# Performance work log

Measured on AMD Instinct MI355X. Metric: run time of the kernel, lower is better.

The kernel has to match this reference:

```python
import jax, jax.numpy as jnp
import numpy as np

N_NODES = 50000
N_EDGES = 800000
IN_FEATS = 96
HIDDEN = 96
OUT_FEATS = 8


def setup_inputs() -> dict:
    key = jax.random.key(0)
    k = jax.random.split(key, 10)
    features = jax.random.normal(k[0], (N_NODES, IN_FEATS), dtype=jnp.float32)
    src = jax.random.randint(k[1], (N_EDGES,), 0, N_NODES, dtype=jnp.int32)
    dst = jax.random.randint(k[2], (N_EDGES,), 0, N_NODES, dtype=jnp.int32)
    # DGL GraphConv weights: shape (in, out), xavier-uniform; bias zeros (we use small randn for nontrivial grads)
    def glorot(kk, fan_in, fan_out):
        lim = np.sqrt(6.0 / (fan_in + fan_out))
        return jax.random.uniform(kk, (fan_in, fan_out), jnp.float32, -lim, lim)
    W1 = glorot(k[3], IN_FEATS, HIDDEN)
    b1 = jnp.zeros((HIDDEN,), jnp.float32)
    W2 = glorot(k[4], HIDDEN, HIDDEN)
    b2 = jnp.zeros((HIDDEN,), jnp.float32)
    # torch Linear readout: weight [out, in], bias [out]
    Wr = glorot(k[5], OUT_FEATS, HIDDEN)
    br = jnp.zeros((OUT_FEATS,), jnp.float32)
    return {"features": features, "src": src, "dst": dst,
            "W1": W1, "b1": b1, "W2": W2, "b2": b2, "Wr": Wr, "br": br}


def _degree_norms(src, dst, n_nodes):
    ones = jnp.ones(src.shape[0], jnp.float32)
    deg_out = jax.ops.segment_sum(ones, src, num_segments=n_nodes)
    deg_in = jax.ops.segment_sum(ones, dst, num_segments=n_nodes)
    norm_out = jnp.clip(deg_out, 1.0, None) ** -0.5  # D_out^{-1/2}
    norm_in = jnp.clip(deg_in, 1.0, None) ** -0.5    # D_in^{-1/2}
    return norm_out, norm_in


def _graph_conv(x, src, dst, norm_out, norm_in, W, b):
    # DGL GraphConv, norm='both': scale src feats, sum-aggregate over edges,
    # scale by in-degree norm, dense transform + bias.
    x = x * norm_out[:, None]
    msgs = x[src]                                           # [E, d] gather
    agg = jax.ops.segment_sum(msgs, dst, num_segments=x.shape[0])  # [N, d] scatter-add
    agg = agg * norm_in[:, None]
    return agg @ W + b


def reference(features, src, dst, W1, b1, W2, b2, Wr, br):
    n = features.shape[0]
    norm_out, norm_in = _degree_norms(src, dst, n)
    x = jax.nn.relu(_graph_conv(features, src, dst, norm_out, norm_in, W1, b1))
    x = _graph_conv(x, src, dst, norm_out, norm_in, W2, b2)
    hg = jnp.mean(x, axis=0, keepdims=True)  # [1, hidden]
    return hg @ Wr.T + br                    # [1, out_feats]
```

## Files before the change

### kernel.cpp

```cpp
#include <hip/hip_runtime.h>


constexpr int NN = 50000;
constexpr int NE = 800000;
constexpr int NB = 196;
constexpr int CAP = 6144;

constexpr int OFF_SVEC     = 0;
constexpr int OFF_BCURD    = 256;
constexpr int OFF_BCURS    = 3392;
constexpr int OFF_NORM_OUT = 6528;
constexpr int OFF_NORM_IN  = 56528;
constexpr int OFF_CW       = 106528;
constexpr int OFF_ROW_PTR  = 156528;
constexpr int OFF_EDGE_SRC = 206532;
constexpr int OFF_PD       = 606532;
constexpr int OFF_PS       = 1810756;
constexpr int OFF_YP       = 606532;
constexpr size_t ZERO_BYTES = (size_t)(OFF_NORM_OUT) * 4;

__global__ __launch_bounds__(256)
void k_part(const int* __restrict__ src, const int* __restrict__ dst,
            int* __restrict__ bcur_d, int* __restrict__ bcur_s,
            int* __restrict__ pd, int* __restrict__ ps) {
  __shared__ int hd[256], hs[256], gd[256], gs[256];
  __shared__ int ldx[256], cur[256], scn[256];
  __shared__ int stage[2048];
  __shared__ unsigned char stageB[2048];
  const int t = threadIdx.x;
  hd[t] = 0; hs[t] = 0;
  __syncthreads();
  const int e0 = blockIdx.x * 2048;
  int s_[8], d_[8];
#pragma unroll
  for (int i = 0; i < 8; ++i) {
    int e = e0 + i * 256 + t;
    bool v = e < NE;
    s_[i] = v ? src[e] : -1;
    d_[i] = v ? dst[e] : -1;
    if (v) { atomicAdd(&hd[d_[i] >> 8], 1); atomicAdd(&hs[s_[i] >> 8], 1); }
  }
  __syncthreads();
  if (t < NB) {
    int c = hd[t];
    gd[t] = c ? (t * CAP + atomicAdd(&bcur_d[t * 16], c)) : 0;
    c = hs[t];
    gs[t] = c ? (t * CAP + atomicAdd(&bcur_s[t * 16], c)) : 0;
  }

  scn[t] = hd[t];
  __syncthreads();
  for (int off = 1; off < 256; off <<= 1) {
    int u = (t >= off) ? scn[t - off] : 0;
    __syncthreads();
    scn[t] += u;
    __syncthreads();
  }
  ldx[t] = scn[t] - hd[t];
  cur[t] = scn[t] - hd[t];
  const int totd = scn[255];
  __syncthreads();
#pragma unroll
  for (int i = 0; i < 8; ++i) {
    if (d_[i] >= 0) {
      int B = d_[i] >> 8;
      int p = atomicAdd(&cur[B], 1);
      stage[p] = (s_[i] << 8) | (d_[i] & 255);
      stageB[p] = (unsigned char)B;
    }
  }
  __syncthreads();
  for (int j = t; j < totd; j += 256) {
    int B = stageB[j];
    pd[gd[B] + (j - ldx[B])] = stage[j];
  }
  __syncthreads();

  scn[t] = hs[t];
  __syncthreads();
  for (int off = 1; off < 256; off <<= 1) {
    int u = (t >= off) ? scn[t - off] : 0;
    __syncthreads();
    scn[t] += u;
    __syncthreads();
  }
  ldx[t] = scn[t] - hs[t];
  cur[t] = scn[t] - hs[t];
  const int tots = scn[255];
  __syncthreads();
#pragma unroll
  for (int i = 0; i < 8; ++i) {
    if (s_[i] >= 0) {
      int B = s_[i] >> 8;
      int p = atomicAdd(&cur[B], 1);
      stage[p] = (d_[i] << 8) | (s_[i] & 255);
      stageB[p] = (unsigned char)B;
    }
  }
  __syncthreads();
  for (int j = t; j < tots; j += 256) {
    int B = stageB[j];
    ps[gs[B] + (j - ldx[B])] = stage[j];
  }
}

__global__ __launch_bounds__(256)
void k_csr(const int* __restrict__ pd, const int* __restrict__ bcur_d,
           int* __restrict__ row_ptr, float* __restrict__ norm_in,
           unsigned short* __restrict__ edge_src) {
  __shared__ int pe_s[CAP];
  __shared__ int hist[256], cur[256], sc[256];
  const int t = threadIdx.x, b = blockIdx.x;
  hist[t] = 0;
  __syncthreads();
  const int cnt = bcur_d[b * 16];
  const int* pe = pd + b * CAP;
  for (int i = t; i < cnt; i += 256) {
    int p = pe[i];
    pe_s[i] = p;
    atomicAdd(&hist[p & 255], 1);
  }

  sc[t] = (t < b) ? bcur_d[t * 16] : 0;
  __syncthreads();
  for (int s = 128; s > 0; s >>= 1) {
    if (t < s) sc[t] += sc[t + s];
    __syncthreads();
  }
  const int base0 = sc[0];
  __syncthreads();

  int h = hist[t];
  sc[t] = h;
  __syncthreads();
  for (int off = 1; off < 256; off <<= 1) {
    int u = (t >= off) ? sc[t - off] : 0;
    __syncthreads();
    sc[t] += u;
    __syncthreads();
  }
  int excl = base0 + sc[t] - h;
  int n = b * 256 + t;
  if (n < NN) {
    row_ptr[n] = excl;
    norm_in[n] = 1.0f / sqrtf((float)max(h, 1));
  }
  cur[t] = excl;
  __syncthreads();
  if (b == NB - 1 && t == 0) row_ptr[NN] = base0 + cnt;

  for (int i = t; i < cnt; i += 256) {
    int p = pe_s[i];
    int pos = atomicAdd(&cur[p & 255], 1);
    edge_src[pos] = (unsigned short)(p >> 8);
  }
}

__global__ __launch_bounds__(256)
void k_bin_src(const int* __restrict__ ps, const int* __restrict__ bcur_s,
               const float* __restrict__ norm_in,
               float* __restrict__ norm_out, float* __restrict__ cw) {
  __shared__ int dout[256];
  __shared__ float craw[256];
  const int t = threadIdx.x, b = blockIdx.x;
  dout[t] = 0; craw[t] = 0.f;
  __syncthreads();
  const int cnt = bcur_s[b * 16];
  const int* pe = ps + b * CAP;
  for (int i = t; i < cnt; i += 256) {
    int p = pe[i];
    atomicAdd(&dout[p & 255], 1);
    atomicAdd(&craw[p & 255], norm_in[p >> 8]);
  }
  __syncthreads();
  int n = b * 256 + t;
  if (n < NN) {
    float no = 1.0f / sqrtf((float)max(dout[t], 1));
    norm_out[n] = no;
    cw[n] = no * craw[t];
  }
}

__global__ __launch_bounds__(256, 6)
void k_xform(const float* __restrict__ feats, const float* __restrict__ norm_out,
             const float* __restrict__ W1, float* __restrict__ YP) {
  __shared__ float XT[96][68];
  const int t = threadIdx.x;
  const int nb = blockIdx.x * 64;

  const float4* f4 = (const float4*)feats;
#pragma unroll
  for (int i = 0; i < 6; ++i) {
    int idx4 = i * 256 + t;
    int n = idx4 / 24;
    int kq = idx4 % 24;
    int ng = nb + n;
    float4 v = make_float4(0.f, 0.f, 0.f, 0.f);
    float no = 0.f;
    if (ng < NN) { v = f4[(size_t)ng * 24 + kq]; no = norm_out[ng]; }
    XT[kq * 4 + 0][n] = v.x * no;
    XT[kq * 4 + 1][n] = v.y * no;
    XT[kq * 4 + 2][n] = v.z * no;
    XT[kq * 4 + 3][n] = v.w * no;
  }
  __syncthreads();

  const int tn = t & 7;
  const int tm = t >> 3;
  float acc0[12], acc1[12];
#pragma unroll
  for (int c = 0; c < 12; ++c) { acc0[c] = 0.f; acc1[c] = 0.f; }

  const float4* W4 = (const float4*)(W1 + 12 * tn);
#pragma unroll 4
  for (int k = 0; k < 96; ++k) {
    float2 x = *(const float2*)&XT[k][2 * tm];
    float4 w0 = W4[k * 24 + 0];
    float4 w1 = W4[k * 24 + 1];
    float4 w2 = W4[k * 24 + 2];
    const float w[12] = {w0.x, w0.y, w0.z, w0.w, w1.x, w1.y, w1.z, w1.w,
                         w2.x, w2.y, w2.z, w2.w};
#pragma unroll
    for (int c = 0; c < 12; ++c) {
      acc0[c] = fmaf(x.x, w[c], acc0[c]);
      acc1[c] = fmaf(x.y, w[c], acc1[c]);
    }
  }

  int n0 = nb + 2 * tm;
#pragma unroll
  for (int c4 = 0; c4 < 3; ++c4) {
    int col = 12 * tn + 4 * c4;
    int p = col >> 4, off = col & 15;
    float* base = YP + ((size_t)p * NN) * 16 + off;
    if (n0 < NN)
      *(float4*)(base + (size_t)n0 * 16) =
          make_float4(acc0[4 * c4], acc0[4 * c4 + 1], acc0[4 * c4 + 2], acc0[4 * c4 + 3]);
    if (n0 + 1 < NN)
      *(float4*)(base + (size_t)(n0 + 1) * 16) =
          make_float4(acc1[4 * c4], acc1[4 * c4 + 1], acc1[4 * c4 + 2], acc1[4 * c4 + 3]);
  }
}

__global__ __launch_bounds__(256, 6)
void k_agg(const float* __restrict__ YP,
           const float* __restrict__ norm_in, const float* __restrict__ cw,
           const int* __restrict__ row_ptr, const unsigned short* __restrict__ edge_src,
           const float* __restrict__ b1, float* __restrict__ svec) {
  __shared__ float red[16];
  const int tid = threadIdx.x;
  if (tid < 16) red[tid] = 0.f;
  __syncthreads();

  const int xcd   = blockIdx.x & 7;
  const int bp    = blockIdx.x >> 3;
  const int panel = (xcd < 6) ? xcd : (xcd - 6);
  const int slotb = (xcd >= 6) ? 256 : 0;
  const int nslot = (panel < 2) ? 512 : 256;
  const int stride = nslot * 8;

  const int g = tid >> 5, l = tid & 31;
  const int ei = l >> 2;
  const int q4 = (l & 3) * 4;

  const float* Yp = YP + (size_t)panel * NN * 16;
  float4 b4 = make_float4(0.f, 0.f, 0.f, 0.f);
  if (l < 4) b4 = ((const float4*)b1)[4 * panel + l];

  float a0 = 0.f, a1 = 0.f, a2 = 0.f, a3 = 0.f;

  const int gid = (slotb + bp) * 8 + g;
  for (int n = gid; n < NN; n += 2 * stride) {
    const int m = n + stride;
    const bool hb = (m < NN);
    int e1a = row_ptr[n + 1], basea = row_ptr[n];
    int e1b = 0, baseb = 0;
    if (hb) { e1b = row_ptr[m + 1]; baseb = row_ptr[m]; }
    float va0 = 0.f, va1 = 0.f, va2 = 0.f, va3 = 0.f;
    float vb0 = 0.f, vb1 = 0.f, vb2 = 0.f, vb3 = 0.f;

    while (basea < e1a || baseb < e1b) {
      int cnta = min(32, e1a - basea);
      int cntb = min(32, e1b - baseb);
      int esa = 0, esb = 0;
      if (basea + l < e1a) esa = edge_src[basea + l] * 16;
      if (baseb + l < e1b) esb = edge_src[baseb + l] * 16;

      if (cnta > 0) {
        int s0 = __shfl(esa, ei, 32);
        float4 f0 = make_float4(0.f, 0.f, 0.f, 0.f);
        if (ei < cnta) f0 = *(const float4*)(Yp + s0 + q4);
        if (cnta > 8) {
          int s1 = __shfl(esa, 8 + ei, 32);
          float4 f1 = make_float4(0.f, 0.f, 0.f, 0.f);
          if (8 + ei < cnta) f1 = *(const float4*)(Yp + s1 + q4);
          f0.x += f1.x; f0.y += f1.y; f0.z += f1.z; f0.w += f1.w;
        }
        if (cnta > 16) {
          int s2 = __shfl(esa, 16 + ei, 32);
          int s3 = __shfl(esa, 24 + ei, 32);
          float4 f2 = make_float4(0.f, 0.f, 0.f, 0.f), f3 = f2;
          if (16 + ei < cnta) f2 = *(const float4*)(Yp + s2 + q4);
          if (24 + ei < cnta) f3 = *(const float4*)(Yp + s3 + q4);
          f0.x += f2.x + f3.x; f0.y += f2.y + f3.y;
          f0.z += f2.z + f3.z; f0.w += f2.w + f3.w;
        }
        va0 += f0.x; va1 += f0.y; va2 += f0.z; va3 += f0.w;
      }
      if (cntb > 0) {
        int s0 = __shfl(esb, ei, 32);
        float4 f0 = make_float4(0.f, 0.f, 0.f, 0.f);
        if (ei < cntb) f0 = *(const float4*)(Yp + s0 + q4);
        if (cntb > 8) {
          int s1 = __shfl(esb, 8 + ei, 32);
          float4 f1 = make_float4(0.f, 0.f, 0.f, 0.f);
          if (8 + ei < cntb) f1 = *(const float4*)(Yp + s1 + q4);
          f0.x += f1.x; f0.y += f1.y; f0.z += f1.z; f0.w += f1.w;
        }
        if (cntb > 16) {
          int s2 = __shfl(esb, 16 + ei, 32);
          int s3 = __shfl(esb, 24 + ei, 32);
          float4 f2 = make_float4(0.f, 0.f, 0.f, 0.f), f3 = f2;
          if (16 + ei < cntb) f2 = *(const float4*)(Yp + s2 + q4);
          if (24 + ei < cntb) f3 = *(const float4*)(Yp + s3 + q4);
          f0.x += f2.x + f3.x; f0.y += f2.y + f3.y;
          f0.z += f2.z + f3.z; f0.w += f2.w + f3.w;
        }
        vb0 += f0.x; vb1 += f0.y; vb2 += f0.z; vb3 += f0.w;
      }
      basea += 32; baseb += 32;
    }

    va0 += __shfl(va0, l + 16, 32); va1 += __shfl(va1, l + 16, 32);
    va2 += __shfl(va2, l + 16, 32); va3 += __shfl(va3, l + 16, 32);
    va0 += __shfl(va0, l + 8, 32);  va1 += __shfl(va1, l + 8, 32);
    va2 += __shfl(va2, l + 8, 32);  va3 += __shfl(va3, l + 8, 32);
    va0 += __shfl(va0, l + 4, 32);  va1 += __shfl(va1, l + 4, 32);
    va2 += __shfl(va2, l + 4, 32);  va3 += __shfl(va3, l + 4, 32);

    vb0 += __shfl(vb0, l + 16, 32); vb1 += __shfl(vb1, l + 16, 32);
    vb2 += __shfl(vb2, l + 16, 32); vb3 += __shfl(vb3, l + 16, 32);
    vb0 += __shfl(vb0, l + 8, 32);  vb1 += __shfl(vb1, l + 8, 32);
    vb2 += __shfl(vb2, l + 8, 32);  vb3 += __shfl(vb3, l + 8, 32);
    vb0 += __shfl(vb0, l + 4, 32);  vb1 += __shfl(vb1, l + 4, 32);
    vb2 += __shfl(vb2, l + 4, 32);  vb3 += __shfl(vb3, l + 4, 32);

    if (l < 4) {
      float ni = norm_in[n], c = cw[n];
      a0 += c * fmaxf(fmaf(ni, va0, b4.x), 0.f);
      a1 += c * fmaxf(fmaf(ni, va1, b4.y), 0.f);
      a2 += c * fmaxf(fmaf(ni, va2, b4.z), 0.f);
      a3 += c * fmaxf(fmaf(ni, va3, b4.w), 0.f);
      if (hb) {
        float nib = norm_in[m], cb = cw[m];
        a0 += cb * fmaxf(fmaf(nib, vb0, b4.x), 0.f);
        a1 += cb * fmaxf(fmaf(nib, vb1, b4.y), 0.f);
        a2 += cb * fmaxf(fmaf(nib, vb2, b4.z), 0.f);
        a3 += cb * fmaxf(fmaf(nib, vb3, b4.w), 0.f);
      }
    }
  }

  if (l < 4) {
    atomicAdd(&red[4 * l + 0], a0);
    atomicAdd(&red[4 * l + 1], a1);
    atomicAdd(&red[4 * l + 2], a2);
    atomicAdd(&red[4 * l + 3], a3);
  }
  __syncthreads();
  if (tid < 16) atomicAdd(&svec[16 * panel + tid], red[tid]);
}

__global__ void k_final(const float* __restrict__ svec,
                        const float* __restrict__ W2, const float* __restrict__ b2,
                        const float* __restrict__ Wr, const float* __restrict__ br,
                        float* __restrict__ out) {
  __shared__ float hg[96];
  int j = threadIdx.x;
  if (j < 96) {
    float acc = b2[j];
    const float invN = 1.0f / (float)NN;
    for (int k = 0; k < 96; ++k)
      acc = fmaf(svec[k] * invN, W2[k * 96 + j], acc);
    hg[j] = acc;
  }
  __syncthreads();
  if (j < 8) {
    float acc = br[j];
    for (int k = 0; k < 96; ++k)
      acc = fmaf(hg[k], Wr[j * 96 + k], acc);
    out[j] = acc;
  }
}

extern "C" void kernel_launch(void* const* d_in, const int* in_sizes, int n_in,
                              void* d_out, int out_size, void* d_ws, size_t ws_size,
                              hipStream_t stream) {
  const float* feats = (const float*)d_in[0];
  const int*   src   = (const int*)d_in[1];
  const int*   dst   = (const int*)d_in[2];
  const float* W1    = (const float*)d_in[3];
  const float* b1    = (const float*)d_in[4];
  const float* W2    = (const float*)d_in[5];
  const float* b2    = (const float*)d_in[6];
  const float* Wr    = (const float*)d_in[7];
  const float* br    = (const float*)d_in[8];
  float* out = (float*)d_out;

  int*   wsi      = (int*)d_ws;
  float* wsf      = (float*)d_ws;
  float* svec     = wsf + OFF_SVEC;
  int*   bcur_d   = wsi + OFF_BCURD;
  int*   bcur_s   = wsi + OFF_BCURS;
  float* norm_out = wsf + OFF_NORM_OUT;
  float* norm_in  = wsf + OFF_NORM_IN;
  float* cw       = wsf + OFF_CW;
  int*   row_ptr  = wsi + OFF_ROW_PTR;
  unsigned short* edge_src = (unsigned short*)(wsi + OFF_EDGE_SRC);
  int*   pd       = wsi + OFF_PD;
  int*   ps       = wsi + OFF_PS;
  float* YP       = wsf + OFF_YP;

  hipMemsetAsync(d_ws, 0, ZERO_BYTES, stream);

  k_part<<<(NE + 2047) / 2048, 256, 0, stream>>>(src, dst, bcur_d, bcur_s, pd, ps);
  k_csr<<<NB, 256, 0, stream>>>(pd, bcur_d, row_ptr, norm_in, edge_src);
  k_bin_src<<<NB, 256, 0, stream>>>(ps, bcur_s, norm_in, norm_out, cw);
  k_xform<<<(NN + 63) / 64, 256, 0, stream>>>(feats, norm_out, W1, YP);
  k_agg<<<2048, 256, 0, stream>>>(YP, norm_in, cw, row_ptr, edge_src, b1, svec);
  k_final<<<1, 128, 0, stream>>>(svec, W2, b2, Wr, br, out);
}
```

Baseline: 219.7 us.

## Aggregate per 256-node bucket with LDS atomic accumulation instead of per-node warp gathers

The aggregation kernel now gives each block one 256-destination bucket for one 16-column panel. Edges are split evenly across 16 slots, and each gathered feature is scatter-added into a padded LDS accumulator using shared atomics. Edge entries are stored as full ints carrying both the source and local destination, which doubles edge array traffic and shifts workspace offsets. This removes per-node load imbalance and the shuffle reductions, at the cost of LDS atomic contention and scalar 4-byte gathers in place of float4 loads.

```diff
diff --git a/kernel.cpp b/kernel.cpp
--- a/kernel.cpp
+++ b/kernel.cpp
@@ -14,9 +14,9 @@
 constexpr int OFF_CW       = 106528;
 constexpr int OFF_ROW_PTR  = 156528;
 constexpr int OFF_EDGE_SRC = 206532;
-constexpr int OFF_PD       = 606532;
-constexpr int OFF_PS       = 1810756;
-constexpr int OFF_YP       = 606532;
+constexpr int OFF_PD       = 1006532;
+constexpr int OFF_PS       = 2210756;
+constexpr int OFF_YP       = 1006532;
 constexpr size_t ZERO_BYTES = (size_t)(OFF_NORM_OUT) * 4;
 
 __global__ __launch_bounds__(256)
@@ -107,7 +107,7 @@
 __global__ __launch_bounds__(256)
 void k_csr(const int* __restrict__ pd, const int* __restrict__ bcur_d,
            int* __restrict__ row_ptr, float* __restrict__ norm_in,
-           unsigned short* __restrict__ edge_src) {
+           int* __restrict__ edge_src) {
   __shared__ int pe_s[CAP];
   __shared__ int hist[256], cur[256], sc[256];
   const int t = threadIdx.x, b = blockIdx.x;
@@ -152,7 +152,7 @@
   for (int i = t; i < cnt; i += 256) {
     int p = pe_s[i];
     int pos = atomicAdd(&cur[p & 255], 1);
-    edge_src[pos] = (unsigned short)(p >> 8);
+    edge_src[pos] = p;
   }
 }
 
@@ -242,133 +242,74 @@
   }
 }
 
-__global__ __launch_bounds__(256, 6)
+__global__ __launch_bounds__(256)
 void k_agg(const float* __restrict__ YP,
            const float* __restrict__ norm_in, const float* __restrict__ cw,
-           const int* __restrict__ row_ptr, const unsigned short* __restrict__ edge_src,
+           const int* __restrict__ row_ptr, const int* __restrict__ edge_src,
            const float* __restrict__ b1, float* __restrict__ svec) {
+  __shared__ float acc[256 * 17];
   __shared__ float red[16];
-  const int tid = threadIdx.x;
-  if (tid < 16) red[tid] = 0.f;
-  __syncthreads();
-
-  const int xcd   = blockIdx.x & 7;
-  const int bp    = blockIdx.x >> 3;
-  const int panel = (xcd < 6) ? xcd : (xcd - 6);
-  const int slotb = (xcd >= 6) ? 256 : 0;
-  const int nslot = (panel < 2) ? 512 : 256;
-  const int stride = nslot * 8;
-
-  const int g = tid >> 5, l = tid & 31;
-  const int ei = l >> 2;
-  const int q4 = (l & 3) * 4;
-
-  const float* Yp = YP + (size_t)panel * NN * 16;
-  float4 b4 = make_float4(0.f, 0.f, 0.f, 0.f);
-  if (l < 4) b4 = ((const float4*)b1)[4 * panel + l];
-
-  float a0 = 0.f, a1 = 0.f, a2 = 0.f, a3 = 0.f;
-
-  const int gid = (slotb + bp) * 8 + g;
-  for (int n = gid; n < NN; n += 2 * stride) {
-    const int m = n + stride;
-    const bool hb = (m < NN);
-    int e1a = row_ptr[n + 1], basea = row_ptr[n];
-    int e1b = 0, baseb = 0;
-    if (hb) { e1b = row_ptr[m + 1]; baseb = row_ptr[m]; }
-    float va0 = 0.f, va1 = 0.f, va2 = 0.f, va3 = 0.f;
-    float vb0 = 0.f, vb1 = 0.f, vb2 = 0.f, vb3 = 0.f;
-
-    while (basea < e1a || baseb < e1b) {
-      int cnta = min(32, e1a - basea);
-      int cntb = min(32, e1b - baseb);
-      int esa = 0, esb = 0;
-      if (basea + l < e1a) esa = edge_src[basea + l] * 16;
-      if (baseb + l < e1b) esb = edge_src[baseb + l] * 16;
-
-      if (cnta > 0) {
-        int s0 = __shfl(esa, ei, 32);
-        float4 f0 = make_float4(0.f, 0.f, 0.f, 0.f);
-        if (ei < cnta) f0 = *(const float4*)(Yp + s0 + q4);
-        if (cnta > 8) {
-          int s1 = __shfl(esa, 8 + ei, 32);
-          float4 f1 = make_float4(0.f, 0.f, 0.f, 0.f);
-          if (8 + ei < cnta) f1 = *(const float4*)(Yp + s1 + q4);
-          f0.x += f1.x; f0.y += f1.y; f0.z += f1.z; f0.w += f1.w;
-        }
-        if (cnta > 16) {
-          int s2 = __shfl(esa, 16 + ei, 32);
-          int s3 = __shfl(esa, 24 + ei, 32);
-          float4 f2 = make_float4(0.f, 0.f, 0.f, 0.f), f3 = f2;
-          if (16 + ei < cnta) f2 = *(const float4*)(Yp + s2 + q4);
-          if (24 + ei < cnta) f3 = *(const float4*)(Yp + s3 + q4);
-          f0.x += f2.x + f3.x; f0.y += f2.y + f3.y;
-          f0.z += f2.z + f3.z; f0.w += f2.w + f3.w;
-        }
-        va0 += f0.x; va1 += f0.y; va2 += f0.z; va3 += f0.w;
-      }
-      if (cntb > 0) {
-        int s0 = __shfl(esb, ei, 32);
-        float4 f0 = make_float4(0.f, 0.f, 0.f, 0.f);
-        if (ei < cntb) f0 = *(const float4*)(Yp + s0 + q4);
-        if (cntb > 8) {
-          int s1 = __shfl(esb, 8 + ei, 32);
-          float4 f1 = make_float4(0.f, 0.f, 0.f, 0.f);
-          if (8 + ei < cntb) f1 = *(const float4*)(Yp + s1 + q4);
-          f0.x += f1.x; f0.y += f1.y; f0.z += f1.z; f0.w += f1.w;
-        }
-        if (cntb > 16) {
-          int s2 = __shfl(esb, 16 + ei, 32);
-          int s3 = __shfl(esb, 24 + ei, 32);
-          float4 f2 = make_float4(0.f, 0.f, 0.f, 0.f), f3 = f2;
-          if (16 + ei < cntb) f2 = *(const float4*)(Yp + s2 + q4);
-          if (24 + ei < cntb) f3 = *(const float4*)(Yp + s3 + q4);
-          f0.x += f2.x + f3.x; f0.y += f2.y + f3.y;
-          f0.z += f2.z + f3.z; f0.w += f2.w + f3.w;
-        }
-        vb0 += f0.x; vb1 += f0.y; vb2 += f0.z; vb3 += f0.w;
-      }
-      basea += 32; baseb += 32;
+  const int t = threadIdx.x;
+  const int x = blockIdx.x & 7, g = blockIdx.x >> 3;
+  int panel, bucket;
+  if (x < 6) {
+    panel = x;
+    if (x < 2) { if (g >= 98) return; bucket = 2 * g; }
+    else       { bucket = g; }
+  } else {
+    panel = x - 6;
+    if (g >= 98) return;
+    bucket = 2 * g + 1;
+  }
+
+  for (int i = t; i < 256 * 17; i += 256) acc[i] = 0.f;
+  if (t < 16) red[t] = 0.f;
+  __syncthreads();
+
+  const int nb = bucket * 256;
+  const int e0 = row_ptr[nb];
+  const int e1 = row_ptr[min(nb + 256, NN)];
+  const float* __restrict__ Yp = YP + (size_t)panel * NN * 16;
+
+  const int slot = t >> 4, col = t & 15;
+  const int cnt = e1 - e0;
+  const int L = (cnt + 15) >> 4;
+  const int i0 = e0 + slot * L;
+  const int iend = min(i0 + L, e1);
+#pragma unroll 4
+  for (int i = i0; i < iend; ++i) {
+    int p = edge_src[i];
+    float v = Yp[(size_t)(p >> 8) * 16 + col];
+    atomicAdd(&acc[(p & 255) * 17 + col], v);
+  }
+  __syncthreads();
+
+  int n = nb + t;
+  float part[16];
+  if (n < NN) {
+    float ni = norm_in[n], c = cw[n];
+#pragma unroll
+    for (int cc = 0; cc < 16; ++cc) {
+      float h = fmaxf(fmaf(ni, acc[t * 17 + cc], b1[16 * panel + cc]), 0.f);
+      part[cc] = c * h;
     }
-
-    va0 += __shfl(va0, l + 16, 32); va1 += __shfl(va1, l + 16, 32);
-    va2 += __shfl(va2, l + 16, 32); va3 += __shfl(va3, l + 16, 32);
-    va0 += __shfl(va0, l + 8, 32);  va1 += __shfl(va1, l + 8, 32);
-    va2 += __shfl(va2, l + 8, 32);  va3 += __shfl(va3, l + 8, 32);
-    va0 += __shfl(va0, l + 4, 32);  va1 += __shfl(va1, l + 4, 32);
-    va2 += __shfl(va2, l + 4, 32);  va3 += __shfl(va3, l + 4, 32);
-
-    vb0 += __shfl(vb0, l + 16, 32); vb1 += __shfl(vb1, l + 16, 32);
-    vb2 += __shfl(vb2, l + 16, 32); vb3 += __shfl(vb3, l + 16, 32);
-    vb0 += __shfl(vb0, l + 8, 32);  vb1 += __shfl(vb1, l + 8, 32);
-    vb2 += __shfl(vb2, l + 8, 32);  vb3 += __shfl(vb3, l + 8, 32);
-    vb0 += __shfl(vb0, l + 4, 32);  vb1 += __shfl(vb1, l + 4, 32);
-    vb2 += __shfl(vb2, l + 4, 32);  vb3 += __shfl(vb3, l + 4, 32);
-
-    if (l < 4) {
-      float ni = norm_in[n], c = cw[n];
-      a0 += c * fmaxf(fmaf(ni, va0, b4.x), 0.f);
-      a1 += c * fmaxf(fmaf(ni, va1, b4.y), 0.f);
-      a2 += c * fmaxf(fmaf(ni, va2, b4.z), 0.f);
-      a3 += c * fmaxf(fmaf(ni, va3, b4.w), 0.f);
-      if (hb) {
-        float nib = norm_in[m], cb = cw[m];
-        a0 += cb * fmaxf(fmaf(nib, vb0, b4.x), 0.f);
-        a1 += cb * fmaxf(fmaf(nib, vb1, b4.y), 0.f);
-        a2 += cb * fmaxf(fmaf(nib, vb2, b4.z), 0.f);
-        a3 += cb * fmaxf(fmaf(nib, vb3, b4.w), 0.f);
-      }
-    }
-  }
-
-  if (l < 4) {
-    atomicAdd(&red[4 * l + 0], a0);
-    atomicAdd(&red[4 * l + 1], a1);
-    atomicAdd(&red[4 * l + 2], a2);
-    atomicAdd(&red[4 * l + 3], a3);
-  }
-  __syncthreads();
-  if (tid < 16) atomicAdd(&svec[16 * panel + tid], red[tid]);
+  } else {
+#pragma unroll
+    for (int cc = 0; cc < 16; ++cc) part[cc] = 0.f;
+  }
+#pragma unroll
+  for (int cc = 0; cc < 16; ++cc) {
+    float v = part[cc];
+    v += __shfl_xor(v, 32);
+    v += __shfl_xor(v, 16);
+    v += __shfl_xor(v, 8);
+    v += __shfl_xor(v, 4);
+    v += __shfl_xor(v, 2);
+    v += __shfl_xor(v, 1);
+    if ((t & 63) == 0) atomicAdd(&red[cc], v);
+  }
+  __syncthreads();
+  if (t < 16) atomicAdd(&svec[16 * panel + t], red[t]);
 }
 
 __global__ void k_final(const float* __restrict__ svec,
@@ -416,7 +357,7 @@
   float* norm_in  = wsf + OFF_NORM_IN;
   float* cw       = wsf + OFF_CW;
   int*   row_ptr  = wsi + OFF_ROW_PTR;
-  unsigned short* edge_src = (unsigned short*)(wsi + OFF_EDGE_SRC);
+  int*   edge_src = wsi + OFF_EDGE_SRC;
   int*   pd       = wsi + OFF_PD;
   int*   ps       = wsi + OFF_PS;
   float* YP       = wsf + OFF_YP;
@@ -427,6 +368,6 @@
   k_csr<<<NB, 256, 0, stream>>>(pd, bcur_d, row_ptr, norm_in, edge_src);
   k_bin_src<<<NB, 256, 0, stream>>>(ps, bcur_s, norm_in, norm_out, cw);
   k_xform<<<(NN + 63) / 64, 256, 0, stream>>>(feats, norm_out, W1, YP);
-  k_agg<<<2048, 256, 0, stream>>>(YP, norm_in, cw, row_ptr, edge_src, b1, svec);
+  k_agg<<<196 * 8, 256, 0, stream>>>(YP, norm_in, cw, row_ptr, edge_src, b1, svec);
   k_final<<<1, 128, 0, stream>>>(svec, W2, b2, Wr, br, out);
 }
```

New measurement: 759.1 us. +245.5%, slower.
